# Performance work log

Measured on AMD Instinct MI355X. Metric: run time of the kernel, lower is better.

Reference implementation:

```python
import jax, jax.numpy as jnp
import numpy as np

XYZ_MIN = -1.0
XYZ_MAX = 1.0
ALPHA_INIT = 0.01
ACT_SHIFT = float(np.log(1.0 / (1.0 - ALPHA_INIT) - 1.0))  # density bias shift
INTERVAL = 0.5  # stepsize * voxel_size_ratio
VIEWBASE_PE = 4


def trilinear(grid, pts):
    """grid: [C,X,Y,Z]; pts: [...,3] in world coords; align_corners=True trilinear."""
    gs = grid.shape[1:]
    size_f = jnp.asarray(gs, pts.dtype)
    u = (pts - XYZ_MIN) / (XYZ_MAX - XYZ_MIN) * (size_f - 1.0)
    u = jnp.clip(u, 0.0, size_f - 1.0)
    i0 = jnp.floor(u).astype(jnp.int32)
    i0 = jnp.minimum(i0, jnp.asarray(gs, jnp.int32) - 2)
    f = u - i0.astype(pts.dtype)
    x0, y0, z0 = i0[..., 0], i0[..., 1], i0[..., 2]
    x1, y1, z1 = x0 + 1, y0 + 1, z0 + 1
    fx, fy, fz = f[..., 0, None], f[..., 1, None], f[..., 2, None]
    g = lambda ix, iy, iz: jnp.moveaxis(grid[:, ix, iy, iz], 0, -1)  # [...,C]
    c00 = g(x0, y0, z0) * (1 - fz) + g(x0, y0, z1) * fz
    c01 = g(x0, y1, z0) * (1 - fz) + g(x0, y1, z1) * fz
    c10 = g(x1, y0, z0) * (1 - fz) + g(x1, y0, z1) * fz
    c11 = g(x1, y1, z0) * (1 - fz) + g(x1, y1, z1) * fz
    c0 = c00 * (1 - fy) + c01 * fy
    c1 = c10 * (1 - fy) + c11 * fy
    return c0 * (1 - fx) + c1 * fx


def setup_inputs() -> dict:
    key = jax.random.key(0)
    ks = jax.random.split(key, 8)
    N, S, G, C, W = 4096, 256, 160, 12, 128
    dim0 = 3 + 3 * VIEWBASE_PE * 2 + C  # 39
    pts = jax.random.uniform(ks[0], (N, S, 3), jnp.float32, minval=-1.0, maxval=1.0)
    viewdirs = jax.random.normal(ks[1], (N, 3), jnp.float32)
    density_grid = jax.random.normal(ks[2], (1, G, G, G), jnp.float32)
    k0_grid = jax.random.normal(ks[3], (C, G, G, G), jnp.float32)
    w0 = jax.random.normal(ks[4], (dim0, W), jnp.float32) * 0.1
    w1 = jax.random.normal(ks[5], (W, W), jnp.float32) * 0.1
    w2 = jax.random.normal(ks[6], (W, 3), jnp.float32) * 0.1
    return dict(pts=pts, viewdirs=viewdirs, density_grid=density_grid, k0_grid=k0_grid,
                w0=w0, b0=jnp.zeros((W,), jnp.float32), w1=w1, b1=jnp.zeros((W,), jnp.float32),
                w2=w2, b2=jnp.zeros((3,), jnp.float32))


def reference(pts, viewdirs, density_grid, k0_grid, w0, b0, w1, b1, w2, b2):
    # --- density query + Raw2Alpha: alpha = 1 - (1+exp(d+shift))^(-interval) ---
    dens = trilinear(density_grid, pts)[..., 0]  # [N,S]
    alpha = 1.0 - jnp.exp(-jax.nn.softplus(dens + ACT_SHIFT) * INTERVAL)
    # --- Alphas2Weights: per-ray exclusive transmittance cumprod ---
    T = jnp.cumprod(1.0 - alpha, axis=1)  # [N,S]
    T_excl = jnp.concatenate([jnp.ones_like(T[:, :1]), T[:, :-1]], axis=1)
    weights = alpha * T_excl  # [N,S]
    alphainv_last = T[:, -1]  # [N]
    # --- color feature grid + view positional encoding ---
    k0 = trilinear(k0_grid, pts)  # [N,S,C]
    vd = viewdirs / jnp.linalg.norm(viewdirs, axis=-1, keepdims=True)  # [N,3]
    freqs = (2.0 ** jnp.arange(VIEWBASE_PE)).astype(vd.dtype)
    vf = (vd[..., None] * freqs).reshape(vd.shape[0], -1)  # [N,12]
    emb = jnp.concatenate([vd, jnp.sin(vf), jnp.cos(vf)], axis=-1)  # [N,27]
    feat = jnp.concatenate(
        [k0, jnp.broadcast_to(emb[:, None, :], k0.shape[:2] + (emb.shape[-1],))], axis=-1)  # [N,S,39]
    # --- rgbnet MLP (depth 3) ---
    h = jax.nn.relu(feat @ w0 + b0)
    h = jax.nn.relu(h @ w1 + b1)
    rgb = jax.nn.sigmoid(h @ w2 + b2)  # [N,S,3]
    # --- composite with white background ---
    rgb_marched = jnp.einsum('ns,nsc->nc', weights, rgb) + alphainv_last[:, None]
    return rgb_marched
```

## Files before the change

kernel.cpp:

```cpp
#include <hip/hip_runtime.h>
#include <hip/hip_fp16.h>

#define G      160
#define G3     (G*G*G)
#define NRAYS  4096
#define SAMP   256
#define CK0    12
#define HID    128

#define ACT_SHIFT (-4.59511985013459f)

#define FS 72
#define HS 136
#define SLABH (64 * HS)

typedef __attribute__((ext_vector_type(8))) _Float16 f16x8;
typedef __attribute__((ext_vector_type(4))) float    f32x4;

__device__ __forceinline__ unsigned pkrtz_u(float a, float b) {
    typedef __attribute__((ext_vector_type(2))) __fp16 fp16v2;
    union { fp16v2 h; unsigned u; } cv;
    cv.h = __builtin_amdgcn_cvt_pkrtz(a, b);
    return cv.u;
}

__global__ __launch_bounds__(256) void prepass_kernel(
        const float* __restrict__ dgrid,
        const float* __restrict__ kgrid,
        unsigned short* __restrict__ vox)
{
    int v4 = (blockIdx.x * 256 + threadIdx.x) * 4;
    if (v4 >= G3) return;
    union F4 { float4 v; float f[4]; };
    F4 d; d.v = *reinterpret_cast<const float4*>(dgrid + v4);
    F4 kk[CK0];
#pragma unroll
    for (int c = 0; c < CK0; c++)
        kk[c].v = *reinterpret_cast<const float4*>(kgrid + (size_t)c * G3 + v4);
#pragma unroll
    for (int i = 0; i < 4; i++) {
        uint4 qa, qb;
        qa.x = pkrtz_u(kk[0].f[i],  kk[1].f[i]);
        qa.y = pkrtz_u(kk[2].f[i],  kk[3].f[i]);
        qa.z = pkrtz_u(kk[4].f[i],  kk[5].f[i]);
        qa.w = pkrtz_u(kk[6].f[i],  kk[7].f[i]);
        qb.x = pkrtz_u(kk[8].f[i],  kk[9].f[i]);
        qb.y = pkrtz_u(kk[10].f[i], kk[11].f[i]);
        qb.z = 0u;
        qb.w = pkrtz_u(0.0f, d.f[i]);
        uint4* dst = reinterpret_cast<uint4*>(vox + (size_t)(v4 + i) * 16);
        dst[0] = qa;
        dst[1] = qb;
    }
}

#define W0PE (16 * 512)
#define W1PE (32 * 512)
#define W2PE (4 * 512)
__global__ __launch_bounds__(256) void pack_weights(
        const float* __restrict__ w0, const float* __restrict__ w1,
        const float* __restrict__ w2,
        unsigned short* __restrict__ w0p, unsigned short* __restrict__ w1p,
        unsigned short* __restrict__ w2p)
{
    int idx = blockIdx.x * 256 + threadIdx.x;
    if (idx < W0PE) {
        int f = idx >> 9, r = idx & 511, l = r >> 3, j = r & 7;
        int nt = f >> 1, ks = f & 1;
        int k = ks * 32 + ((l >> 4) << 3) + j;
        int nn = nt * 16 + (l & 15);
        w0p[idx] = (k < 39) ? __half_as_ushort(__float2half(w0[k * HID + nn]))
                            : (unsigned short)0;
    } else if (idx < W0PE + W1PE) {
        int m = idx - W0PE;
        int f = m >> 9, r = m & 511, l = r >> 3, j = r & 7;
        int nt = f >> 2, ks = f & 3;
        int k = ks * 32 + ((l >> 4) << 3) + j;
        int nn = nt * 16 + (l & 15);
        w1p[m] = __half_as_ushort(__float2half(w1[k * HID + nn]));
    } else if (idx < W0PE + W1PE + W2PE) {
        int m = idx - W0PE - W1PE;
        int ks = m >> 9, r = m & 511, l = r >> 3, j = r & 7;
        int k = ks * 32 + ((l >> 4) << 3) + j;
        int nn = l & 15;
        w2p[m] = (nn < 3) ? __half_as_ushort(__float2half(w2[k * 3 + nn]))
                          : (unsigned short)0;
    }
}

__global__ __launch_bounds__(256) void dvgo_mfma(
        const float* __restrict__ pts,
        const float* __restrict__ viewdirs,
        const unsigned short* __restrict__ vox,
        const unsigned short* __restrict__ w0p,
        const unsigned short* __restrict__ w1p,
        const unsigned short* __restrict__ w2p,
        const float* __restrict__ b0, const float* __restrict__ b1,
        const float* __restrict__ b2,
        float* __restrict__ out)
{
    __shared__ __half s_mem[4 * SLABH];
    __shared__ float  s_wgt[SAMP];
    __shared__ float  s_wave[4];
    __shared__ unsigned s_u[16];
    __shared__ float  s_out[4];

    const int n    = blockIdx.x;
    const int t    = threadIdx.x;
    const int lane = t & 63;
    const int wv   = t >> 6;
    const int wbase = wv << 6;
    const int c    = lane & 15;
    const int quad = lane >> 4;
    __half* slab = s_mem + wv * SLABH;
    const int lr = lane;

    if (t < 4) s_out[t] = 0.0f;

    if (t < 14) {
        float v0 = viewdirs[n * 3 + 0];
        float v1 = viewdirs[n * 3 + 1];
        float v2 = viewdirs[n * 3 + 2];
        float inv = rsqrtf(v0 * v0 + v1 * v1 + v2 * v2);
        float vd[3] = {v0 * inv, v1 * inv, v2 * inv};
        float fv[2];
#pragma unroll
        for (int e = 0; e < 2; e++) {
            int col = 12 + 2 * t + e;
            float f;
            if (col < 15)      f = vd[col - 12];
            else if (col < 27) { int s = col - 15; f = __sinf(vd[s >> 2] * (float)(1 << (s & 3))); }
            else if (col < 39) { int s = col - 27; f = __cosf(vd[s >> 2] * (float)(1 << (s & 3))); }
            else               f = 0.0f;
            fv[e] = f;
        }
        s_u[t + 2] = pkrtz_u(fv[0], fv[1]);
    }

    const float* p = pts + ((size_t)n * SAMP + t) * 3;
    float pc[3] = {p[0], p[1], p[2]};
    int   i0[3];
    float fr[3];
#pragma unroll
    for (int d = 0; d < 3; d++) {
        float uu = (pc[d] + 1.0f) * 0.5f * (float)(G - 1);
        uu = fminf(fmaxf(uu, 0.0f), (float)(G - 1));
        int i = (int)floorf(uu);
        if (i > G - 2) i = G - 2;
        i0[d] = i;
        fr[d] = uu - (float)i;
    }

    __half2 accA0 = __float2half2_rn(0.0f), accA1 = accA0, accA2 = accA0, accA3 = accA0;
    __half2 accB0 = accA0, accB1 = accA0;
    float dens = 0.0f;

#pragma unroll
    for (int cx = 0; cx < 2; cx++) {
        float wx = cx ? fr[0] : 1.0f - fr[0];
#pragma unroll
        for (int cy = 0; cy < 2; cy++) {
            float wxy = wx * (cy ? fr[1] : 1.0f - fr[1]);
#pragma unroll
            for (int cz = 0; cz < 2; cz++) {
                float w = wxy * (cz ? fr[2] : 1.0f - fr[2]);
                int vidx = ((i0[0] + cx) * G + (i0[1] + cy)) * G + (i0[2] + cz);
                const uint4* q = reinterpret_cast<const uint4*>(vox) + (size_t)vidx * 2;
                union { uint4 q; __half2 h2[4]; } A, B;
                A.q = q[0];
                B.q = q[1];
                __half2 wh = __half2half2(__float2half(w));
                accA0 = __hfma2(wh, A.h2[0], accA0);
                accA1 = __hfma2(wh, A.h2[1], accA1);
                accA2 = __hfma2(wh, A.h2[2], accA2);
                accA3 = __hfma2(wh, A.h2[3], accA3);
                accB0 = __hfma2(wh, B.h2[0], accB0);
                accB1 = __hfma2(wh, B.h2[1], accB1);
                dens += w * __half2float(__high2half(B.h2[3]));
            }
        }
    }

    float xs = dens + ACT_SHIFT;
    float sp = fmaxf(xs, 0.0f) + __logf(1.0f + __expf(-fabsf(xs)));
    float alpha = 1.0f - __expf(-sp * 0.5f);

    float xi = 1.0f - alpha;
#pragma unroll
    for (int off = 1; off < 64; off <<= 1) {
        float y = __shfl_up(xi, off);
        if (lane >= off) xi *= y;
    }
    if (lane == 63) s_wave[wv] = xi;

    __syncthreads();

    float prefix = 1.0f;
#pragma unroll
    for (int u = 0; u < 3; u++)
        if (u < wv) prefix *= s_wave[u];
    float xp = __shfl_up(xi, 1);
    float Texcl = prefix * ((lane == 0) ? 1.0f : xp);
    s_wgt[t] = alpha * Texcl;

    {
        uint4 q0, q1;
        union { __half2 h; unsigned u; } cv;
        cv.h = accA0; q0.x = cv.u;
        cv.h = accA1; q0.y = cv.u;
        cv.h = accA2; q0.z = cv.u;
        cv.h = accA3; q0.w = cv.u;
        cv.h = accB0; q1.x = cv.u;
        cv.h = accB1; q1.y = cv.u;
        q1.z = s_u[2];
        q1.w = s_u[3];
        *reinterpret_cast<uint4*>(slab + lr * FS)     = q0;
        *reinterpret_cast<uint4*>(slab + lr * FS + 8) = q1;
        const uint4* uq = reinterpret_cast<const uint4*>(s_u);
        *reinterpret_cast<uint4*>(slab + lr * FS + 16) = uq[1];
        *reinterpret_cast<uint4*>(slab + lr * FS + 24) = uq[2];
        *reinterpret_cast<uint4*>(slab + lr * FS + 32) = uq[3];
    }

    const f32x4 zf = {0.0f, 0.0f, 0.0f, 0.0f};
    const f16x8 zfrag = {};

    f16x8 a1[4][2];
#pragma unroll
    for (int mt = 0; mt < 4; mt++) {
        a1[mt][0] = *reinterpret_cast<const f16x8*>(slab + (mt * 16 + c) * FS + quad * 8);
        a1[mt][1] = zfrag;
        if (quad == 0)
            a1[mt][1] = *reinterpret_cast<const f16x8*>(slab + (mt * 16 + c) * FS + 32);
    }

    const uint4* w0q = reinterpret_cast<const uint4*>(w0p);
#pragma unroll
    for (int nt = 0; nt < 8; nt++) {
        union { uint4 q; f16x8 s; } bA, bB;
        bA.q = w0q[(nt * 2 + 0) * 64 + lane];
        bB.q = w0q[(nt * 2 + 1) * 64 + lane];
        f32x4 acc[4];
#pragma unroll
        for (int mt = 0; mt < 4; mt++) {
            f32x4 tmp = __builtin_amdgcn_mfma_f32_16x16x32_f16(a1[mt][0], bA.s, zf, 0, 0, 0);
            acc[mt]   = __builtin_amdgcn_mfma_f32_16x16x32_f16(a1[mt][1], bB.s, tmp, 0, 0, 0);
        }
        float bias = b0[nt * 16 + c];
#pragma unroll
        for (int mt = 0; mt < 4; mt++)
#pragma unroll
            for (int r = 0; r < 4; r++)
                slab[(mt * 16 + quad * 4 + r) * HS + nt * 16 + c] =
                    __float2half(fmaxf(acc[mt][r] + bias, 0.0f));
    }

    f16x8 a2[4][4];
#pragma unroll
    for (int mt = 0; mt < 4; mt++)
#pragma unroll
        for (int ks = 0; ks < 4; ks++)
            a2[mt][ks] = *reinterpret_cast<const f16x8*>(
                slab + (mt * 16 + c) * HS + ks * 32 + quad * 8);

    const uint4* w1q = reinterpret_cast<const uint4*>(w1p);
#pragma unroll
    for (int nt = 0; nt < 8; nt++) {
        f32x4 acc[4] = {zf, zf, zf, zf};
#pragma unroll
        for (int ks = 0; ks < 4; ks++) {
            union { uint4 q; f16x8 s; } bb;
            bb.q = w1q[(nt * 4 + ks) * 64 + lane];
#pragma unroll
            for (int mt = 0; mt < 4; mt++)
                acc[mt] = __builtin_amdgcn_mfma_f32_16x16x32_f16(a2[mt][ks], bb.s, acc[mt], 0, 0, 0);
        }
        float bias = b1[nt * 16 + c];
#pragma unroll
        for (int mt = 0; mt < 4; mt++)
#pragma unroll
            for (int r = 0; r < 4; r++)
                slab[(mt * 16 + quad * 4 + r) * HS + nt * 16 + c] =
                    __float2half(fmaxf(acc[mt][r] + bias, 0.0f));
    }

    f16x8 a3[4][4];
#pragma unroll
    for (int mt = 0; mt < 4; mt++)
#pragma unroll
        for (int ks = 0; ks < 4; ks++)
            a3[mt][ks] = *reinterpret_cast<const f16x8*>(
                slab + (mt * 16 + c) * HS + ks * 32 + quad * 8);

    const uint4* w2q = reinterpret_cast<const uint4*>(w2p);
    f32x4 acc3[4] = {zf, zf, zf, zf};
#pragma unroll
    for (int ks = 0; ks < 4; ks++) {
        union { uint4 q; f16x8 s; } bb;
        bb.q = w2q[ks * 64 + lane];
#pragma unroll
        for (int mt = 0; mt < 4; mt++)
            acc3[mt] = __builtin_amdgcn_mfma_f32_16x16x32_f16(a3[mt][ks], bb.s, acc3[mt], 0, 0, 0);
    }

    float b2c = (c < 3) ? b2[c] : 0.0f;
    float csum = 0.0f;
#pragma unroll
    for (int mt = 0; mt < 4; mt++)
#pragma unroll
        for (int r = 0; r < 4; r++) {
            int m = wbase + mt * 16 + quad * 4 + r;
            float pre = acc3[mt][r] + b2c;
            float sg = 1.0f / (1.0f + __expf(-pre));
            csum += s_wgt[m] * sg;
        }
    csum += __shfl_xor(csum, 16);
    csum += __shfl_xor(csum, 32);
    if (quad == 0 && c < 3) atomicAdd(&s_out[c], csum);

    __syncthreads();
    if (t < 3) {
        float alast = s_wave[0] * s_wave[1] * s_wave[2] * s_wave[3];
        out[n * 3 + t] = s_out[t] + alast;
    }
}

__global__ __launch_bounds__(256, 2) void dvgo_fallback(
        const float* __restrict__ pts, const float* __restrict__ viewdirs,
        const float* __restrict__ dgrid, const float* __restrict__ kgrid,
        const float* __restrict__ w0, const float* __restrict__ b0,
        const float* __restrict__ w1, const float* __restrict__ b1,
        const float* __restrict__ w2, const float* __restrict__ b2,
        float* __restrict__ out)
{
    const int n = blockIdx.x;
    const int t = threadIdx.x;
    __shared__ float s_alpha[SAMP];
    __shared__ float s_P[SAMP];
    __shared__ float s_red[12];

    const float* p = pts + ((size_t)n * SAMP + t) * 3;
    float pc[3] = {p[0], p[1], p[2]};
    int i0[3]; float fr[3];
#pragma unroll
    for (int d = 0; d < 3; d++) {
        float uu = (pc[d] + 1.0f) * 0.5f * (float)(G - 1);
        uu = fminf(fmaxf(uu, 0.0f), (float)(G - 1));
        int i = (int)floorf(uu);
        if (i > G - 2) i = G - 2;
        i0[d] = i; fr[d] = uu - (float)i;
    }
    float dens = 0.0f, k0v[CK0];
#pragma unroll
    for (int ch = 0; ch < CK0; ch++) k0v[ch] = 0.0f;
#pragma unroll
    for (int cx = 0; cx < 2; cx++)
#pragma unroll
        for (int cy = 0; cy < 2; cy++)
#pragma unroll
            for (int cz = 0; cz < 2; cz++) {
                float w = (cx ? fr[0] : 1.0f - fr[0]) * (cy ? fr[1] : 1.0f - fr[1]) * (cz ? fr[2] : 1.0f - fr[2]);
                int vidx = ((i0[0] + cx) * G + (i0[1] + cy)) * G + (i0[2] + cz);
                dens += w * dgrid[vidx];
#pragma unroll
                for (int ch = 0; ch < CK0; ch++) k0v[ch] += w * kgrid[(size_t)ch * G3 + vidx];
            }
    float xs = dens + ACT_SHIFT;
    float sp = (xs > 20.0f) ? xs : log1pf(expf(xs));
    float alpha = 1.0f - expf(-sp * 0.5f);
    s_alpha[t] = alpha; s_P[t] = 1.0f - alpha;
    __syncthreads();
#pragma unroll
    for (int off = 1; off < SAMP; off <<= 1) {
        float v = (t >= off) ? s_P[t - off] : 1.0f;
        __syncthreads();
        s_P[t] *= v;
        __syncthreads();
    }
    float v0 = viewdirs[n * 3 + 0], v1 = viewdirs[n * 3 + 1], v2 = viewdirs[n * 3 + 2];
    float inv = 1.0f / sqrtf(v0 * v0 + v1 * v1 + v2 * v2);
    v0 *= inv; v1 *= inv; v2 *= inv;
    float feat[39];
#pragma unroll
    for (int ch = 0; ch < CK0; ch++) feat[ch] = k0v[ch];
    feat[12] = v0; feat[13] = v1; feat[14] = v2;
    float vd3[3] = {v0, v1, v2};
#pragma unroll
    for (int i = 0; i < 3; i++)
#pragma unroll
        for (int j = 0; j < 4; j++) {
            float a = vd3[i] * (float)(1 << j);
            feat[15 + i * 4 + j] = sinf(a);
            feat[27 + i * 4 + j] = cosf(a);
        }
    float h1[HID];
#pragma unroll 1
    for (int ch = 0; ch < 4; ch++) {
        float acc[32];
#pragma unroll
        for (int j = 0; j < 32; j++) acc[j] = b0[ch * 32 + j];
#pragma unroll
        for (int k = 0; k < 39; k++) {
            float f = feat[k];
#pragma unroll
            for (int j = 0; j < 32; j++) acc[j] = fmaf(f, w0[k * HID + ch * 32 + j], acc[j]);
        }
#pragma unroll
        for (int j = 0; j < 32; j++) h1[ch * 32 + j] = fmaxf(acc[j], 0.0f);
    }
    float rgbpre[3] = {b2[0], b2[1], b2[2]};
#pragma unroll 1
    for (int ch = 0; ch < 4; ch++) {
        float acc[32];
#pragma unroll
        for (int j = 0; j < 32; j++) acc[j] = b1[ch * 32 + j];
#pragma unroll 4
        for (int k = 0; k < HID; k++) {
            float hk = h1[k];
#pragma unroll
            for (int j = 0; j < 32; j++) acc[j] = fmaf(hk, w1[k * HID + ch * 32 + j], acc[j]);
        }
#pragma unroll
        for (int j = 0; j < 32; j++) {
            float h2 = fmaxf(acc[j], 0.0f);
            int jj = ch * 32 + j;
            rgbpre[0] = fmaf(h2, w2[jj * 3 + 0], rgbpre[0]);
            rgbpre[1] = fmaf(h2, w2[jj * 3 + 1], rgbpre[1]);
            rgbpre[2] = fmaf(h2, w2[jj * 3 + 2], rgbpre[2]);
        }
    }
    float T_excl = (t == 0) ? 1.0f : s_P[t - 1];
    float wgt = s_alpha[t] * T_excl;
    float c0 = wgt / (1.0f + expf(-rgbpre[0]));
    float c1 = wgt / (1.0f + expf(-rgbpre[1]));
    float c2 = wgt / (1.0f + expf(-rgbpre[2]));
#pragma unroll
    for (int off = 32; off > 0; off >>= 1) {
        c0 += __shfl_down(c0, off);
        c1 += __shfl_down(c1, off);
        c2 += __shfl_down(c2, off);
    }
    if ((t & 63) == 0) {
        int wvv = t >> 6;
        s_red[wvv * 3 + 0] = c0; s_red[wvv * 3 + 1] = c1; s_red[wvv * 3 + 2] = c2;
    }
    __syncthreads();
    if (t == 0) {
        float alast = s_P[SAMP - 1];
        float o0 = alast, o1 = alast, o2 = alast;
#pragma unroll
        for (int wvv = 0; wvv < 4; wvv++) {
            o0 += s_red[wvv * 3 + 0]; o1 += s_red[wvv * 3 + 1]; o2 += s_red[wvv * 3 + 2];
        }
        out[n * 3 + 0] = o0; out[n * 3 + 1] = o1; out[n * 3 + 2] = o2;
    }
}

extern "C" void kernel_launch(void* const* d_in, const int* in_sizes, int n_in,
                              void* d_out, int out_size, void* d_ws, size_t ws_size,
                              hipStream_t stream) {
    const float* pts      = (const float*)d_in[0];
    const float* viewdirs = (const float*)d_in[1];
    const float* dgrid    = (const float*)d_in[2];
    const float* kgrid    = (const float*)d_in[3];
    const float* w0       = (const float*)d_in[4];
    const float* b0       = (const float*)d_in[5];
    const float* w1       = (const float*)d_in[6];
    const float* b1       = (const float*)d_in[7];
    const float* w2       = (const float*)d_in[8];
    const float* b2       = (const float*)d_in[9];
    float* out = (float*)d_out;

    const size_t VOXB = (size_t)G3 * 32;
    const size_t TOTB = VOXB + (size_t)(W0PE + W1PE + W2PE) * 2;

    if (ws_size >= TOTB) {
        unsigned short* vox  = (unsigned short*)d_ws;
        unsigned short* w0pp = (unsigned short*)((char*)d_ws + VOXB);
        unsigned short* w1pp = w0pp + W0PE;
        unsigned short* w2pp = w1pp + W1PE;
        prepass_kernel<<<G3 / 4 / 256, 256, 0, stream>>>(dgrid, kgrid, vox);
        pack_weights<<<(W0PE + W1PE + W2PE + 255) / 256, 256, 0, stream>>>(
            w0, w1, w2, w0pp, w1pp, w2pp);
        dvgo_mfma<<<NRAYS, 256, 0, stream>>>(pts, viewdirs, vox, w0pp, w1pp, w2pp,
                                             b0, b1, b2, out);
    } else {
        dvgo_fallback<<<NRAYS, SAMP, 0, stream>>>(pts, viewdirs, dgrid, kgrid,
                                                  w0, b0, w1, b1, w2, b2, out);
    }
}
```

Baseline: 519.7 us.

## Drop voxel repack prepass and gather directly from fp32 planar grids

Removes the prepass kernel that repacked the density and 12-channel feature grids into an interleaved fp16 voxel layout every call. The main kernel now gathers from the original fp32 planar grids, reading z and z+1 pairs per channel and accumulating in fp32. This avoids writing and re-reading a roughly 130 MB packed buffer on each call. In exchange, each sample makes many scattered 4-byte loads across 13 separate planes instead of two 16-byte loads per corner, which reduces cache-line locality during the gather.

```diff
diff --git a/kernel.cpp b/kernel.cpp
--- a/kernel.cpp
+++ b/kernel.cpp
@@ -22,36 +22,6 @@
     union { fp16v2 h; unsigned u; } cv;
     cv.h = __builtin_amdgcn_cvt_pkrtz(a, b);
     return cv.u;
-}
-
-__global__ __launch_bounds__(256) void prepass_kernel(
-        const float* __restrict__ dgrid,
-        const float* __restrict__ kgrid,
-        unsigned short* __restrict__ vox)
-{
-    int v4 = (blockIdx.x * 256 + threadIdx.x) * 4;
-    if (v4 >= G3) return;
-    union F4 { float4 v; float f[4]; };
-    F4 d; d.v = *reinterpret_cast<const float4*>(dgrid + v4);
-    F4 kk[CK0];
-#pragma unroll
-    for (int c = 0; c < CK0; c++)
-        kk[c].v = *reinterpret_cast<const float4*>(kgrid + (size_t)c * G3 + v4);
-#pragma unroll
-    for (int i = 0; i < 4; i++) {
-        uint4 qa, qb;
-        qa.x = pkrtz_u(kk[0].f[i],  kk[1].f[i]);
-        qa.y = pkrtz_u(kk[2].f[i],  kk[3].f[i]);
-        qa.z = pkrtz_u(kk[4].f[i],  kk[5].f[i]);
-        qa.w = pkrtz_u(kk[6].f[i],  kk[7].f[i]);
-        qb.x = pkrtz_u(kk[8].f[i],  kk[9].f[i]);
-        qb.y = pkrtz_u(kk[10].f[i], kk[11].f[i]);
-        qb.z = 0u;
-        qb.w = pkrtz_u(0.0f, d.f[i]);
-        uint4* dst = reinterpret_cast<uint4*>(vox + (size_t)(v4 + i) * 16);
-        dst[0] = qa;
-        dst[1] = qb;
-    }
 }
 
 #define W0PE (16 * 512)
@@ -91,7 +61,8 @@
 __global__ __launch_bounds__(256) void dvgo_mfma(
         const float* __restrict__ pts,
         const float* __restrict__ viewdirs,
-        const unsigned short* __restrict__ vox,
+        const float* __restrict__ dgrid,
+        const float* __restrict__ kgrid,
         const unsigned short* __restrict__ w0p,
         const unsigned short* __restrict__ w1p,
         const unsigned short* __restrict__ w2p,
@@ -151,9 +122,11 @@
         fr[d] = uu - (float)i;
     }
 
-    __half2 accA0 = __float2half2_rn(0.0f), accA1 = accA0, accA2 = accA0, accA3 = accA0;
-    __half2 accB0 = accA0, accB1 = accA0;
+    float k0v[CK0];
+#pragma unroll
+    for (int ch = 0; ch < CK0; ch++) k0v[ch] = 0.0f;
     float dens = 0.0f;
+    const float fz = fr[2], ifz = 1.0f - fz;
 
 #pragma unroll
     for (int cx = 0; cx < 2; cx++) {
@@ -161,22 +134,14 @@
 #pragma unroll
         for (int cy = 0; cy < 2; cy++) {
             float wxy = wx * (cy ? fr[1] : 1.0f - fr[1]);
-#pragma unroll
-            for (int cz = 0; cz < 2; cz++) {
-                float w = wxy * (cz ? fr[2] : 1.0f - fr[2]);
-                int vidx = ((i0[0] + cx) * G + (i0[1] + cy)) * G + (i0[2] + cz);
-                const uint4* q = reinterpret_cast<const uint4*>(vox) + (size_t)vidx * 2;
-                union { uint4 q; __half2 h2[4]; } A, B;
-                A.q = q[0];
-                B.q = q[1];
-                __half2 wh = __half2half2(__float2half(w));
-                accA0 = __hfma2(wh, A.h2[0], accA0);
-                accA1 = __hfma2(wh, A.h2[1], accA1);
-                accA2 = __hfma2(wh, A.h2[2], accA2);
-                accA3 = __hfma2(wh, A.h2[3], accA3);
-                accB0 = __hfma2(wh, B.h2[0], accB0);
-                accB1 = __hfma2(wh, B.h2[1], accB1);
-                dens += w * __half2float(__high2half(B.h2[3]));
+            int base = ((i0[0] + cx) * G + (i0[1] + cy)) * G + i0[2];
+            float d0 = dgrid[base], d1 = dgrid[base + 1];
+            dens += wxy * (d0 * ifz + d1 * fz);
+#pragma unroll
+            for (int ch = 0; ch < CK0; ch++) {
+                float v0 = kgrid[(size_t)ch * G3 + base];
+                float v1 = kgrid[(size_t)ch * G3 + base + 1];
+                k0v[ch] += wxy * (v0 * ifz + v1 * fz);
             }
         }
     }
@@ -205,13 +170,12 @@
 
     {
         uint4 q0, q1;
-        union { __half2 h; unsigned u; } cv;
-        cv.h = accA0; q0.x = cv.u;
-        cv.h = accA1; q0.y = cv.u;
-        cv.h = accA2; q0.z = cv.u;
-        cv.h = accA3; q0.w = cv.u;
-        cv.h = accB0; q1.x = cv.u;
-        cv.h = accB1; q1.y = cv.u;
+        q0.x = pkrtz_u(k0v[0],  k0v[1]);
+        q0.y = pkrtz_u(k0v[2],  k0v[3]);
+        q0.z = pkrtz_u(k0v[4],  k0v[5]);
+        q0.w = pkrtz_u(k0v[6],  k0v[7]);
+        q1.x = pkrtz_u(k0v[8],  k0v[9]);
+        q1.y = pkrtz_u(k0v[10], k0v[11]);
         q1.z = s_u[2];
         q1.w = s_u[3];
         *reinterpret_cast<uint4*>(slab + lr * FS)     = q0;
@@ -471,19 +435,16 @@
     const float* b2       = (const float*)d_in[9];
     float* out = (float*)d_out;
 
-    const size_t VOXB = (size_t)G3 * 32;
-    const size_t TOTB = VOXB + (size_t)(W0PE + W1PE + W2PE) * 2;
+    const size_t TOTB = (size_t)(W0PE + W1PE + W2PE) * 2;
 
     if (ws_size >= TOTB) {
-        unsigned short* vox  = (unsigned short*)d_ws;
-        unsigned short* w0pp = (unsigned short*)((char*)d_ws + VOXB);
+        unsigned short* w0pp = (unsigned short*)d_ws;
         unsigned short* w1pp = w0pp + W0PE;
         unsigned short* w2pp = w1pp + W1PE;
-        prepass_kernel<<<G3 / 4 / 256, 256, 0, stream>>>(dgrid, kgrid, vox);
         pack_weights<<<(W0PE + W1PE + W2PE + 255) / 256, 256, 0, stream>>>(
             w0, w1, w2, w0pp, w1pp, w2pp);
-        dvgo_mfma<<<NRAYS, 256, 0, stream>>>(pts, viewdirs, vox, w0pp, w1pp, w2pp,
-                                             b0, b1, b2, out);
+        dvgo_mfma<<<NRAYS, 256, 0, stream>>>(pts, viewdirs, dgrid, kgrid,
+                                             w0pp, w1pp, w2pp, b0, b1, b2, out);
     } else {
         dvgo_fallback<<<NRAYS, SAMP, 0, stream>>>(pts, viewdirs, dgrid, kgrid,
                                                   w0, b0, w1, b1, w2, b2, out);
```

Result: slower. 1.252 ms (+141.0%).
